# Performance work log

Hardware: AMD Instinct MI355X
Metric: run time of the kernel (lower is better)

## Reference

```python
import jax, jax.numpy as jnp
import numpy as np

TEMP = 0.02
KD_W = 1.0
VSD_W = 1.0
VLAD_W = 1.0
CON_W = 1.0
MSE_W = 1.0

B, SS, ST, DS, DT, V, NV, NT = 8, 96, 128, 1024, 2048, 32000, 32, 64


def hungarian(cost):
    # Shortest-augmenting-path assignment (e-maxx / Jonker-Volgenant style).
    # Square cost [n, n]; returns col_of_row so that row i matches column
    # col_of_row[i] with minimal total cost (same as scipy linear_sum_assignment).
    cost = np.asarray(cost, dtype=np.float64)
    n = cost.shape[0]
    INF = 1e18
    u = np.zeros(n + 1)
    v = np.zeros(n + 1)
    p = np.zeros(n + 1, dtype=np.int64)
    way = np.zeros(n + 1, dtype=np.int64)
    for i in range(1, n + 1):
        p[0] = i
        j0 = 0
        minv = np.full(n + 1, INF)
        used = np.zeros(n + 1, dtype=bool)
        while True:
            used[j0] = True
            i0 = p[j0]
            js = np.nonzero(~used)[0]
            js = js[js > 0]
            cur = cost[i0 - 1, js - 1] - u[i0] - v[js]
            upd = cur < minv[js]
            minv[js] = np.where(upd, cur, minv[js])
            way[js] = np.where(upd, j0, way[js])
            k = int(np.argmin(minv[js]))
            delta = minv[js][k]
            j1 = int(js[k])
            u[p[used]] += delta
            v[used] -= delta
            minv[~used] -= delta
            j0 = j1
            if p[j0] == 0:
                break
        while j0:
            j1 = int(way[j0])
            p[j0] = p[j1]
            j0 = j1
    col_of_row = np.zeros(n, dtype=np.int64)
    for j in range(1, n + 1):
        col_of_row[p[j] - 1] = j - 1
    return col_of_row


def _match(s_logits, t_logits):
    # Per-sample L1 (p=1 cdist) cost between teacher rows and student cols,
    # then Hungarian matching. Host-side loop is unavoidable (sequential
    # combinatorial algorithm), matching the original per-sample scipy loop.
    idx = []
    for b in range(s_logits.shape[0]):
        cost = np.abs(t_logits[b][:, None, :] - s_logits[b][None, :, :]).sum(-1)
        idx.append(hungarian(cost))
    return np.stack(idx)


def _cosine(a, b, eps=1e-8):
    # a: [B, M, D], b: [B, N, D] -> [B, M, N]; torch F.cosine_similarity semantics
    an = a / jnp.maximum(jnp.linalg.norm(a, axis=-1, keepdims=True), eps)
    bn = b / jnp.maximum(jnp.linalg.norm(b, axis=-1, keepdims=True), eps)
    return jnp.einsum('bmd,bnd->bmn', an, bn)


def setup_inputs() -> dict:
    key = jax.random.key(0)
    ks = jax.random.split(key, 12)
    f = jax.random.normal
    return {
        's_qry_reps': f(ks[0], (B, DS), jnp.float32),
        's_pos_reps': f(ks[1], (B, DS), jnp.float32),
        't_qry_reps': f(ks[2], (B, DT), jnp.float32),
        't_pos_reps': f(ks[3], (B, DT), jnp.float32),
        's_hidden_qry': f(ks[4], (B, SS, DS), jnp.float32),
        's_hidden_pos': f(ks[5], (B, SS, DS), jnp.float32),
        't_hidden_qry': f(ks[6], (B, ST, DT), jnp.float32),
        't_hidden_pos': f(ks[7], (B, ST, DT), jnp.float32),
        'W_s_lm': f(ks[8], (DS, V), jnp.float32) / np.float32(np.sqrt(DS)),
        'W_t_lm': f(ks[9], (DT, V), jnp.float32) / np.float32(np.sqrt(DT)),
        'W_proj': f(ks[10], (DT, DS), jnp.float32) / np.float32(np.sqrt(DT)),
        'b_proj': jnp.zeros((DS,), jnp.float32),
        'nv': NV,
        'nt': NT,
    }


def reference(s_qry_reps, s_pos_reps, t_qry_reps, t_pos_reps,
              s_hidden_qry, s_hidden_pos, t_hidden_qry, t_hidden_pos,
              W_s_lm, W_t_lm, W_proj, b_proj, nv, nt):
    Bn = s_qry_reps.shape[0]
    # 1) contrastive InfoNCE (world_size=1 -> gather is identity, target=arange)
    scores = (s_qry_reps @ s_pos_reps.T) / TEMP
    logp = jax.nn.log_softmax(scores, axis=-1)
    contrastive = -jnp.mean(jnp.diagonal(logp))
    # 2) MSE vs t2s-projected teacher reps
    mse = 0.5 * (jnp.mean((s_qry_reps - (t_qry_reps @ W_proj + b_proj)) ** 2)
                 + jnp.mean((s_pos_reps - (t_pos_reps @ W_proj + b_proj)) ** 2))
    # 3/4) VSD + VLAD over qry and pos sides stacked -> [2B, ...]
    s_hid = jnp.concatenate([s_hidden_qry, s_hidden_pos], axis=0)
    t_hid = jnp.concatenate([t_hidden_qry, t_hidden_pos], axis=0)
    St = t_hid.shape[1]
    sv = s_hid[:, :nv]                      # student vision tokens   [2B, Nv, DS]
    st = s_hid[:, nv:nv + nt]               # student text tokens     [2B, Nt, DS]
    tv = t_hid[:, St - nv - nt:St - nt]     # teacher vision tokens   [2B, Nv, DT]
    tt = t_hid[:, St - nt:]                 # teacher text tokens     [2B, Nt, DT]
    s_logits = jnp.einsum('bnd,dv->bnv', sv, W_s_lm)   # [2B, Nv, V]
    t_logits = jnp.einsum('bnd,dv->bnv', tv, W_t_lm)   # [2B, Nv, V]
    # Hungarian matching on detached logits (host side, like the original)
    idx = jnp.asarray(_match(np.asarray(s_logits), np.asarray(t_logits)))  # [2B, Nv]
    # VSD: MSE between matched student logits and teacher logits (t order = arange)
    s_logits_m = jnp.take_along_axis(s_logits, idx[:, :, None], axis=1)
    vsd = jnp.sum(jnp.mean((s_logits_m - t_logits) ** 2, axis=(1, 2)))
    # VLAD: smooth-L1 on vision->text cosine affinity maps
    sv_m = jnp.take_along_axis(sv, idx[:, :, None], axis=1)
    d = _cosine(sv_m, st) - _cosine(tv, tt)            # [2B, Nv, Nt]
    ad = jnp.abs(d)
    sl1 = jnp.where(ad < 1.0, 0.5 * d * d, ad - 0.5)
    vlad = jnp.sum(jnp.mean(sl1, axis=(1, 2)))
    distill = (VSD_W * vsd + VLAD_W * vlad) / Bn
    loss = CON_W * contrastive + MSE_W * mse + KD_W * distill
    return loss, contrastive, distill
```

## Files before the change

### kernel.cpp

```cpp
#include <hip/hip_runtime.h>
#include <math.h>

#define DS_ 1024
#define DT_ 2048
#define V_  32000
#define SS_ 96
#define ST_ 128


__device__ __forceinline__ float block_reduce_sum_256(float v) {
  __shared__ float tmp[4];
  #pragma unroll
  for (int off = 32; off; off >>= 1) v += __shfl_xor(v, off);
  const int wid = threadIdx.x >> 6;
  if ((threadIdx.x & 63) == 0) tmp[wid] = v;
  __syncthreads();
  if (threadIdx.x == 0) v = tmp[0] + tmp[1] + tmp[2] + tmp[3];
  return v;
}

__device__ __forceinline__ const float* s_base(int b, const float* s_hq, const float* s_hp) {
  return (b < 8) ? (s_hq + (size_t)b * SS_ * DS_) : (s_hp + (size_t)(b - 8) * SS_ * DS_);
}
__device__ __forceinline__ const float* t_base(int b, const float* t_hq, const float* t_hp) {
  return (b < 8) ? (t_hq + (size_t)b * ST_ * DT_) : (t_hp + (size_t)(b - 8) * ST_ * DT_);
}

__device__ __forceinline__ unsigned short f2bf(float x) {
  unsigned int u = __float_as_uint(x);
  u += 0x7fffu + ((u >> 16) & 1u);
  return (unsigned short)(u >> 16);
}
__device__ __forceinline__ float bf2f(unsigned short u) {
  return __uint_as_float(((unsigned int)u) << 16);
}

using bf16x8 = __attribute__((ext_vector_type(8))) short;
using f32x4  = __attribute__((ext_vector_type(4))) float;
using u16x4  = __attribute__((ext_vector_type(4))) unsigned short;

__device__ __forceinline__ void gll16(const void* g, void* l) {
  __builtin_amdgcn_global_load_lds((const __attribute__((address_space(1))) unsigned int*)g,
                                   (__attribute__((address_space(3))) unsigned int*)l, 16, 0, 0);
}

__device__ __forceinline__ unsigned int wave_umin_dpp(unsigned int r) {
  unsigned int t;
  t = (unsigned int)__builtin_amdgcn_update_dpp((int)r, (int)r, 0x111, 0xF, 0xF, false); r = r < t ? r : t;
  t = (unsigned int)__builtin_amdgcn_update_dpp((int)r, (int)r, 0x112, 0xF, 0xF, false); r = r < t ? r : t;
  t = (unsigned int)__builtin_amdgcn_update_dpp((int)r, (int)r, 0x114, 0xF, 0xF, false); r = r < t ? r : t;
  t = (unsigned int)__builtin_amdgcn_update_dpp((int)r, (int)r, 0x118, 0xF, 0xF, false); r = r < t ? r : t;
  t = (unsigned int)__builtin_amdgcn_update_dpp((int)r, (int)r, 0x142, 0xF, 0xF, false); r = r < t ? r : t;
  t = (unsigned int)__builtin_amdgcn_update_dpp((int)r, (int)r, 0x143, 0xF, 0xF, false); r = r < t ? r : t;
  return r;
}


__global__ __launch_bounds__(256) void scores_kernel(const float* __restrict__ sq,
                                                     const float* __restrict__ sp,
                                                     float* __restrict__ scores) {
  const int i = blockIdx.x >> 3, j = blockIdx.x & 7;
  float acc = 0.f;
  for (int k = threadIdx.x; k < DS_; k += 256)
    acc += sq[(size_t)i * DS_ + k] * sp[(size_t)j * DS_ + k];
  acc = block_reduce_sum_256(acc);
  if (threadIdx.x == 0) scores[i * 8 + j] = acc * 50.0f;
}


__global__ __launch_bounds__(256) void proj2_kernel(const float* __restrict__ t_qry,
                                                    const float* __restrict__ t_pos,
                                                    const float* __restrict__ Wp,
                                                    float* __restrict__ proj) {
  __shared__ float tv[16][64];
  const int kc = blockIdx.x;
  const int tid = threadIdx.x;
  for (int s = tid; s < 16 * 64; s += 256) {
    const int zi = s >> 6, k = s & 63;
    const float* t = (zi >= 8) ? (t_pos + (size_t)(zi - 8) * DT_) : (t_qry + (size_t)zi * DT_);
    tv[zi][k] = t[kc * 64 + k];
  }
  __syncthreads();
  const int d4 = tid * 4;
  float4 acc[16];
  #pragma unroll
  for (int zi = 0; zi < 16; ++zi) acc[zi] = (float4){0.f, 0.f, 0.f, 0.f};
  for (int k = 0; k < 64; ++k) {
    const float4 w = *(const float4*)&Wp[(size_t)(kc * 64 + k) * DS_ + d4];
    #pragma unroll
    for (int zi = 0; zi < 16; ++zi) {
      const float t = tv[zi][k];
      acc[zi].x += t * w.x; acc[zi].y += t * w.y;
      acc[zi].z += t * w.z; acc[zi].w += t * w.w;
    }
  }
  #pragma unroll
  for (int zi = 0; zi < 16; ++zi) {
    float* p = proj + (size_t)zi * DS_ + d4;
    atomicAdd(&p[0], acc[zi].x); atomicAdd(&p[1], acc[zi].y);
    atomicAdd(&p[2], acc[zi].z); atomicAdd(&p[3], acc[zi].w);
  }
}


__global__ __launch_bounds__(256) void mse2_kernel(const float* __restrict__ s_qry,
                                                   const float* __restrict__ s_pos,
                                                   const float* __restrict__ proj,
                                                   const float* __restrict__ bp,
                                                   float* __restrict__ mse_acc) {
  const int z = blockIdx.x >> 3, i = blockIdx.x & 7;
  const float* s = (z ? s_pos : s_qry) + (size_t)i * DS_;
  const float* p = proj + ((size_t)z * 8 + i) * DS_;
  float ss = 0.f;
  for (int d = threadIdx.x; d < DS_; d += 256) {
    const float diff = s[d] - (p[d] + bp[d]);
    ss += diff * diff;
  }
  ss = block_reduce_sum_256(ss);
  if (threadIdx.x == 0) atomicAdd(mse_acc, ss);
}


__global__ __launch_bounds__(256) void pack_as_kernel(const float* __restrict__ s_hq,
                                                      const float* __restrict__ s_hp,
                                                      unsigned short* __restrict__ As) {
  const int g = blockIdx.x;
  const int b = g >> 5, i = g & 31;
  const float* src = s_base(b, s_hq, s_hp) + (size_t)i * DS_;
  const int k4 = threadIdx.x * 4;
  const float4 w = *(const float4*)&src[k4];
  u16x4 o; o[0] = f2bf(w.x); o[1] = f2bf(w.y); o[2] = f2bf(w.z); o[3] = f2bf(w.w);
  *(u16x4*)&As[(size_t)g * DS_ + k4] = o;
}

__global__ __launch_bounds__(256) void pack_at_kernel(const float* __restrict__ t_hq,
                                                      const float* __restrict__ t_hp,
                                                      unsigned short* __restrict__ At) {
  const int g = blockIdx.x;
  const int b = g >> 5, i = g & 31;
  const float* src = t_base(b, t_hq, t_hp) + (size_t)(32 + i) * DT_;
  #pragma unroll
  for (int it = 0; it < 2; ++it) {
    const int k4 = (threadIdx.x + it * 256) * 4;
    const float4 w = *(const float4*)&src[k4];
    u16x4 o; o[0] = f2bf(w.x); o[1] = f2bf(w.y); o[2] = f2bf(w.z); o[3] = f2bf(w.w);
    *(u16x4*)&At[(size_t)g * DT_ + k4] = o;
  }
}

__global__ __launch_bounds__(256) void convw_kernel(const float* __restrict__ W,
                                                    unsigned short* __restrict__ Wbt,
                                                    int K) {
  __shared__ float tile[64][65];
  const int v0 = blockIdx.x * 64, k0 = blockIdx.y * 64;
  const int tid = threadIdx.x;
  #pragma unroll
  for (int it = 0; it < 4; ++it) {
    const int kr = (tid >> 4) + it * 16;
    const int v4 = (tid & 15) * 4;
    const float4 w = *(const float4*)&W[(size_t)(k0 + kr) * V_ + v0 + v4];
    tile[v4 + 0][kr] = w.x; tile[v4 + 1][kr] = w.y;
    tile[v4 + 2][kr] = w.z; tile[v4 + 3][kr] = w.w;
  }
  __syncthreads();
  #pragma unroll
  for (int it = 0; it < 2; ++it) {
    const int s = tid + it * 256;
    const int v = s >> 3, ch = s & 7;
    const float* src = &tile[v][ch * 8];
    unsigned int o[4];
    #pragma unroll
    for (int q = 0; q < 4; ++q)
      o[q] = (unsigned int)f2bf(src[2 * q]) | ((unsigned int)f2bf(src[2 * q + 1]) << 16);
    uint4 pk = {o[0], o[1], o[2], o[3]};
    *(uint4*)&Wbt[(size_t)(v0 + v) * K + k0 + ch * 8] = pk;
  }
}


template <int K>
__global__ __launch_bounds__(256) void gemm_tn_kernel(const unsigned short* __restrict__ A,
                                                      const unsigned short* __restrict__ Wbt,
                                                      unsigned short* __restrict__ Out) {
  __shared__ __align__(16) unsigned short Alds[2][256 * 32];
  __shared__ __align__(16) unsigned short Blds[2][128 * 32];
  const int nwg = gridDim.x;
  const int q = nwg >> 3, r = nwg & 7;
  const int xcd = blockIdx.x & 7, off = blockIdx.x >> 3;
  const int blk = (xcd < r ? xcd * (q + 1) : r * (q + 1) + (xcd - r) * q) + off;
  const int m0 = (blk & 1) * 256;
  const int n0 = (blk >> 1) * 128;
  const int tid = threadIdx.x;
  const int wv = tid >> 6, lane = tid & 63;
  const int lr = lane & 15, cc = lane >> 4;

  f32x4 acc[4][8];
  #pragma unroll
  for (int mf = 0; mf < 4; ++mf)
    #pragma unroll
    for (int nf = 0; nf < 8; ++nf) acc[mf][nf] = (f32x4){0.f, 0.f, 0.f, 0.f};

  constexpr int NT = K / 32;

  auto stage = [&](int kt, int buf) {
    #pragma unroll
    for (int it = 0; it < 4; ++it) {
      const int slot = it * 256 + tid;
      const int row = slot >> 2, cs = slot & 3;
      gll16(A + (size_t)(m0 + row) * K + kt * 32 + ((cs ^ ((row >> 1) & 3)) << 3),
            Alds[buf] + (size_t)(it * 256 + wv * 64) * 8);
    }
    #pragma unroll
    for (int it = 0; it < 2; ++it) {
      const int slot = it * 256 + tid;
      const int row = slot >> 2, cs = slot & 3;
      gll16(Wbt + (size_t)(n0 + row) * K + kt * 32 + ((cs ^ ((row >> 1) & 3)) << 3),
            Blds[buf] + (size_t)(it * 256 + wv * 64) * 8);
    }
  };

  stage(0, 0);
  if (NT > 1) stage(1, 1);
  for (int kt = 0; kt < NT; ++kt) {
    const int cur = kt & 1;
    if (kt >= 1 && kt + 1 < NT) stage(kt + 1, cur ^ 1);
    if (kt + 1 < NT) asm volatile("s_waitcnt vmcnt(6)" ::: "memory");
    else             asm volatile("s_waitcnt vmcnt(0)" ::: "memory");
    asm volatile("s_barrier" ::: "memory");
    bf16x8 af[4];
    #pragma unroll
    for (int mf = 0; mf < 4; ++mf) {
      const int row = wv * 64 + mf * 16 + lr;
      af[mf] = *(const bf16x8*)(Alds[cur] + row * 32 + ((cc ^ ((row >> 1) & 3)) << 3));
    }
    __builtin_amdgcn_s_setprio(1);
    #pragma unroll
    for (int nf = 0; nf < 8; ++nf) {
      const int vr = nf * 16 + lr;
      const bf16x8 bfr = *(const bf16x8*)(Blds[cur] + vr * 32 + ((cc ^ ((vr >> 1) & 3)) << 3));
      #pragma unroll
      for (int mf = 0; mf < 4; ++mf)
        acc[mf][nf] = __builtin_amdgcn_mfma_f32_16x16x32_bf16(af[mf], bfr, acc[mf][nf], 0, 0, 0);
    }
    __builtin_amdgcn_s_setprio(0);
    asm volatile("s_barrier" ::: "memory");
  }

  unsigned short* Olds = &Alds[0][0];
  #pragma unroll
  for (int h = 0; h < 2; ++h) {
    if (h) __syncthreads();
    #pragma unroll
    for (int mf = 0; mf < 4; ++mf)
      #pragma unroll
      for (int nf4 = 0; nf4 < 4; ++nf4) {
        const int nf = h * 4 + nf4;
        #pragma unroll
        for (int q2 = 0; q2 < 4; ++q2) {
          const int row = wv * 64 + mf * 16 + (lane >> 4) * 4 + q2;
          const int col = nf4 * 16 + lr;
          Olds[row * 64 + (col ^ (((row >> 2) & 3) << 4))] = f2bf(acc[mf][nf][q2]);
        }
      }
    __syncthreads();
    #pragma unroll
    for (int it = 0; it < 4; ++it) {
      const int slot = it * 256 + tid;
      const int row = slot >> 3, c2 = slot & 7;
      const uint4 pk = *(const uint4*)&Olds[row * 64 + ((c2 ^ (((row >> 2) & 3) << 1)) << 3)];
      *(uint4*)&Out[(size_t)(m0 + row) * V_ + n0 + h * 64 + c2 * 8] = pk;
    }
  }
}


#define CPV 500
#define CPP 508

__global__ __launch_bounds__(256) void cost_pairs_kernel(const unsigned short* __restrict__ Sg,
                                                         const unsigned short* __restrict__ Tg,
                                                         float* __restrict__ cost1,
                                                         float* __restrict__ cost2) {
  __shared__ __align__(16) unsigned short Sl[32 * CPP];
  __shared__ __align__(16) unsigned short Tl[32 * CPP];
  const int b = blockIdx.x >> 6, sl = blockIdx.x & 63;
  const int v0 = sl * CPV;
  const int tid = threadIdx.x;

  for (int s = tid; s < 32 * 125; s += 256) {
    const int r = s / 125, c = s % 125;
    *(u16x4*)&Sl[r * CPP + c * 4] = *(const u16x4*)&Sg[(size_t)(b * 32 + r) * V_ + v0 + c * 4];
    *(u16x4*)&Tl[r * CPP + c * 4] = *(const u16x4*)&Tg[(size_t)(b * 32 + r) * V_ + v0 + c * 4];
  }
  __syncthreads();

  const int i = tid >> 3, j4 = (tid & 7) * 4;
  float a1[4] = {0.f, 0.f, 0.f, 0.f}, a2[4] = {0.f, 0.f, 0.f, 0.f};
  for (int v = 0; v < CPV; v += 4) {
    const u16x4 t4 = *(const u16x4*)&Tl[i * CPP + v];
    float tf[4];
    #pragma unroll
    for (int q = 0; q < 4; ++q) tf[q] = bf2f(t4[q]);
    #pragma unroll
    for (int jj = 0; jj < 4; ++jj) {
      const u16x4 s4 = *(const u16x4*)&Sl[(j4 + jj) * CPP + v];
      #pragma unroll
      for (int q = 0; q < 4; ++q) {
        const float d = tf[q] - bf2f(s4[q]);
        a1[jj] += fabsf(d);
        a2[jj] += d * d;
      }
    }
  }
  #pragma unroll
  for (int jj = 0; jj < 4; ++jj) {
    atomicAdd(&cost1[(size_t)b * 1024 + i * 32 + j4 + jj], a1[jj]);
    atomicAdd(&cost2[(size_t)b * 1024 + i * 32 + j4 + jj], a2[jj]);
  }
}


__global__ __launch_bounds__(64) void hungarian_kernel(const float* __restrict__ cost1,
                                                       const float* __restrict__ cost2,
                                                       int* __restrict__ idx,
                                                       float* __restrict__ vsd_acc) {
  const int b = blockIdx.x;
  const int lane = threadIdx.x;
  const float INF = __int_as_float(0x7f800000);
  __shared__ float C[32 * 33];
  __shared__ float u_lds[33];

  for (int s = lane; s < 1024; s += 64) {
    const int r = s >> 5, c = s & 31;
    C[r * 33 + c] = cost1[(size_t)b * 1024 + s];
  }
  if (lane == 0) u_lds[0] = 0.f;
  __syncthreads();

  const bool isj = (lane >= 1 && lane <= 32);
  const int cix = isj ? (lane - 1) : 0;

  if (lane < 32) {
    float m = C[lane * 33];
    for (int j = 1; j < 32; ++j) m = fminf(m, C[lane * 33 + j]);
    u_lds[lane + 1] = m;
  }
  __syncthreads();

  float v = 0.f;
  if (isj) {
    float m = INF;
    for (int i = 0; i < 32; ++i) m = fminf(m, C[i * 33 + cix] - u_lds[i + 1]);
    v = m;
  }

  int p = 0;
  unsigned int assigned = 0;
  for (int i = 1; i <= 32; ++i) {
    const float ui = u_lds[i];
    const bool zero = isj && (p == 0) && ((C[(i - 1) * 33 + cix] - ui) == v);
    const unsigned long long tie = __ballot(zero);
    if (tie) {
      const int j1 = __ffsll(tie) - 1;
      if (lane == j1) p = i;
      assigned |= (1u << (i - 1));
    }
  }

  for (int i = 1; i <= 32; ++i) {
    if (assigned & (1u << (i - 1))) continue;
    if (lane == 0) p = i;
    float minv = INF;
    int way = 0;
    int used = 0;
    int j0 = 0;
    float ui0 = u_lds[i];
    float crow = C[(i - 1) * 33 + cix];
    while (true) {
      if (lane == j0) used = 1;
      float val = INF;
      if (isj && !used) {
        const float cur = crow - ui0 - v;
        if (cur < minv) { minv = cur; way = j0; }
        val = minv;
      }
      const unsigned int rb = wave_umin_dpp(__float_as_uint(val));
      const unsigned int minb = (unsigned int)__builtin_amdgcn_readlane((int)rb, 63);
      const float delta = __uint_as_float(minb);
      const unsigned long long tie = __ballot(__float_as_uint(val) == minb);
      const int j1 = __ffsll(tie) - 1;
      const int i0n = __builtin_amdgcn_readlane(p, j1);
      const float ui0n = u_lds[i0n];
      const int nri = (i0n >= 1 ? i0n : 1) - 1;
      const float cnext = C[nri * 33 + cix];
      if (used) {
        u_lds[p] += delta;
        v -= delta;
      } else {
        minv -= delta;
      }
      j0 = j1;
      if (i0n == 0) break;
      ui0 = ui0n;
      crow = cnext;
    }
    while (j0) {
      const int j1 = __builtin_amdgcn_readlane(way, j0);
      const int pv = __builtin_amdgcn_readlane(p, j1);
      if (lane == j0) p = pv;
      j0 = j1;
    }
  }
  float term = 0.f;
  if (isj) {
    idx[b * 32 + (p - 1)] = lane - 1;
    term = cost2[(size_t)b * 1024 + (p - 1) * 32 + (lane - 1)];
  }
  #pragma unroll
  for (int off = 32; off; off >>= 1) term += __shfl_xor(term, off);
  if (lane == 0) atomicAdd(vsd_acc, term);
}


__global__ __launch_bounds__(256) void norms_kernel(const float* __restrict__ s_hq,
                                                    const float* __restrict__ s_hp,
                                                    const float* __restrict__ t_hq,
                                                    const float* __restrict__ t_hp,
                                                    float* __restrict__ invn) {
  const int blk = blockIdx.x;
  const int b = blk / 192, t = blk % 192;
  const float* bs = s_base(b, s_hq, s_hp);
  const float* bt = t_base(b, t_hq, t_hp);
  const float* row;
  int K;
  float* out;
  if (t < 32)       { row = bs + (size_t)t * DS_;             K = DS_; out = invn + b * 32 + t; }
  else if (t < 96)  { row = bs + (size_t)t * DS_;             K = DS_; out = invn + 512 + b * 64 + (t - 32); }
  else if (t < 128) { row = bt + (size_t)(t - 96 + 32) * DT_;  K = DT_; out = invn + 1536 + b * 32 + (t - 96); }
  else              { row = bt + (size_t)(t - 128 + 64) * DT_; K = DT_; out = invn + 2048 + b * 64 + (t - 128); }
  float ss = 0.f;
  for (int k = threadIdx.x; k < K; k += 256) { const float x = row[k]; ss += x * x; }
  ss = block_reduce_sum_256(ss);
  if (threadIdx.x == 0) *out = 1.0f / fmaxf(sqrtf(ss), 1e-8f);
}


__global__ __launch_bounds__(256) void vlad_kernel2(const float* __restrict__ s_hq,
                                                    const float* __restrict__ s_hp,
                                                    const float* __restrict__ t_hq,
                                                    const float* __restrict__ t_hp,
                                                    const int* __restrict__ idx,
                                                    const float* __restrict__ invn,
                                                    float* __restrict__ vlad_acc) {
  const int b = blockIdx.x >> 5, i = blockIdx.x & 31;
  const int wv = threadIdx.x >> 6, lane = threadIdx.x & 63;
  const float* bs = s_base(b, s_hq, s_hp);
  const float* bt = t_base(b, t_hq, t_hp);
  const int is = idx[b * 32 + i];
  const float* a1p = bs + (size_t)is * DS_;
  const float* a2p = bt + (size_t)(32 + i) * DT_;
  float a1[16], a2[32];
  #pragma unroll
  for (int q = 0; q < 16; ++q) a1[q] = a1p[lane + 64 * q];
  #pragma unroll
  for (int q = 0; q < 32; ++q) a2[q] = a2p[lane + 64 * q];
  const float in_s = invn[b * 32 + is];
  const float in_t = invn[1536 + b * 32 + i];
  float local = 0.f;
  for (int jj = 0; jj < 16; ++jj) {
    const int j = wv * 16 + jj;
    const float* b1 = bs + (size_t)(32 + j) * DS_;
    const float* b2 = bt + (size_t)(64 + j) * DT_;
    float ds = 0.f, dt = 0.f;
    #pragma unroll
    for (int q = 0; q < 16; ++q) ds += a1[q] * b1[lane + 64 * q];
    #pragma unroll
    for (int q = 0; q < 32; ++q) dt += a2[q] * b2[lane + 64 * q];
    #pragma unroll
    for (int off = 32; off; off >>= 1) {
      ds += __shfl_xor(ds, off);
      dt += __shfl_xor(dt, off);
    }
    if (lane == 0) {
      const float cs = ds * in_s * invn[512 + b * 64 + j];
      const float ct = dt * in_t * invn[2048 + b * 64 + j];
      const float d = cs - ct;
      const float ad = fabsf(d);
      local += (ad < 1.f) ? 0.5f * d * d : ad - 0.5f;
    }
  }
  if (lane == 0) atomicAdd(vlad_acc, local);
}


__global__ __launch_bounds__(64) void final_kernel(const float* __restrict__ scores,
                                                   const float* __restrict__ accs,
                                                   float* __restrict__ out) {
  const int lane = threadIdx.x;
  float ci = 0.f;
  if (lane < 8) {
    float m = -1e30f;
    for (int j = 0; j < 8; ++j) m = fmaxf(m, scores[lane * 8 + j]);
    float sum = 0.f;
    for (int j = 0; j < 8; ++j) sum += expf(scores[lane * 8 + j] - m);
    const float lse = m + logf(sum);
    ci = scores[lane * 8 + lane] - lse;
  }
  #pragma unroll
  for (int off = 32; off; off >>= 1) ci += __shfl_xor(ci, off);
  if (lane == 0) {
    const float contrastive = -ci / 8.0f;
    const float mse = accs[0] / 16384.0f;
    const float vsd = accs[1] / 1024000.0f;
    const float vlad = accs[2] / 2048.0f;
    const float distill = (vsd + vlad) / 8.0f;
    out[0] = contrastive + mse + distill;
    out[1] = contrastive;
    out[2] = distill;
  }
}


extern "C" void kernel_launch(void* const* d_in, const int* in_sizes, int n_in,
                              void* d_out, int out_size, void* d_ws, size_t ws_size,
                              hipStream_t stream) {
  const float* s_qry = (const float*)d_in[0];
  const float* s_pos = (const float*)d_in[1];
  const float* t_qry = (const float*)d_in[2];
  const float* t_pos = (const float*)d_in[3];
  const float* s_hq  = (const float*)d_in[4];
  const float* s_hp  = (const float*)d_in[5];
  const float* t_hq  = (const float*)d_in[6];
  const float* t_hp  = (const float*)d_in[7];
  const float* Ws    = (const float*)d_in[8];
  const float* Wt    = (const float*)d_in[9];
  const float* Wp    = (const float*)d_in[10];
  const float* bp    = (const float*)d_in[11];

  float* ws     = (float*)d_ws;
  float* scores = ws;
  float* cost1  = ws + 64;
  float* cost2  = ws + 16448;
  float* invn   = ws + 32832;
  float* accs   = ws + 35904;
  float* proj   = ws + 35908;
  int*   idx    = (int*)(ws + 52292);
  const size_t small_bytes = (size_t)(52292 + 512) * 4;

  const size_t As_off = 262144;
  const size_t At_off = As_off + (size_t)512 * DS_ * 2;
  const size_t Ws_off = At_off + (size_t)512 * DT_ * 2;
  const size_t Wt_off = Ws_off + (size_t)V_ * DS_ * 2;
  const size_t Sg_off = Wt_off + (size_t)V_ * DT_ * 2;
  const size_t Tg_off = Sg_off + (size_t)512 * V_ * 2;
  const size_t req2   = Tg_off + (size_t)512 * V_ * 2;

  hipMemsetAsync(d_ws, 0, small_bytes, stream);

  scores_kernel<<<64, 256, 0, stream>>>(s_qry, s_pos, scores);
  proj2_kernel<<<32, 256, 0, stream>>>(t_qry, t_pos, Wp, proj);
  mse2_kernel<<<16, 256, 0, stream>>>(s_qry, s_pos, proj, bp, accs + 0);
  norms_kernel<<<16 * 192, 256, 0, stream>>>(s_hq, s_hp, t_hq, t_hp, invn);

  if (ws_size >= req2) {
    unsigned short* As  = (unsigned short*)((char*)d_ws + As_off);
    unsigned short* At  = (unsigned short*)((char*)d_ws + At_off);
    unsigned short* Wsb = (unsigned short*)((char*)d_ws + Ws_off);
    unsigned short* Wtb = (unsigned short*)((char*)d_ws + Wt_off);
    unsigned short* Sg  = (unsigned short*)((char*)d_ws + Sg_off);
    unsigned short* Tg  = (unsigned short*)((char*)d_ws + Tg_off);
    pack_as_kernel<<<512, 256, 0, stream>>>(s_hq, s_hp, As);
    pack_at_kernel<<<512, 256, 0, stream>>>(t_hq, t_hp, At);
    convw_kernel<<<dim3(V_ / 64, DS_ / 64), 256, 0, stream>>>(Ws, Wsb, DS_);
    convw_kernel<<<dim3(V_ / 64, DT_ / 64), 256, 0, stream>>>(Wt, Wtb, DT_);
    gemm_tn_kernel<DS_><<<(V_ / 128) * 2, 256, 0, stream>>>(As, Wsb, Sg);
    gemm_tn_kernel<DT_><<<(V_ / 128) * 2, 256, 0, stream>>>(At, Wtb, Tg);
    cost_pairs_kernel<<<16 * 64, 256, 0, stream>>>(Sg, Tg, cost1, cost2);
  }

  hungarian_kernel<<<16, 64, 0, stream>>>(cost1, cost2, idx, accs + 1);
  vlad_kernel2<<<512, 256, 0, stream>>>(s_hq, s_hp, t_hq, t_hp, idx, invn, accs + 2);
  final_kernel<<<1, 64, 0, stream>>>(scores, accs, (float*)d_out);
}
```

Measured before the change: 508.1 us.

## Fuse prep and mid-stage kernels into multi-role launches and precompute teacher cosines

Merges scores, projection, norms, packing and the student weight conversion into one heterogeneous kernel indexed by block range. A second kernel runs the student GEMM, the teacher weight conversion and the teacher cosine dot products side by side. The teacher vision-text cosine matrix is computed once, before the Hungarian step, so the VLAD kernel only has to do the student side. This removes several launch gaps and runs independent work concurrently, at the cost of larger shared-memory reservations per block and uneven block roles. The final kernels now also sit inside the workspace-size branch.

Result: faster. 463.8 us (-8.7%).

```diff
diff --git a/kernel.cpp b/kernel.cpp
--- a/kernel.cpp
+++ b/kernel.cpp
@@ -56,10 +56,10 @@
 }
 
 
-__global__ __launch_bounds__(256) void scores_kernel(const float* __restrict__ sq,
-                                                     const float* __restrict__ sp,
-                                                     float* __restrict__ scores) {
-  const int i = blockIdx.x >> 3, j = blockIdx.x & 7;
+__device__ __forceinline__ void scores_body(int blk, const float* __restrict__ sq,
+                                            const float* __restrict__ sp,
+                                            float* __restrict__ scores) {
+  const int i = blk >> 3, j = blk & 7;
   float acc = 0.f;
   for (int k = threadIdx.x; k < DS_; k += 256)
     acc += sq[(size_t)i * DS_ + k] * sp[(size_t)j * DS_ + k];
@@ -67,13 +67,12 @@
   if (threadIdx.x == 0) scores[i * 8 + j] = acc * 50.0f;
 }
 
-
-__global__ __launch_bounds__(256) void proj2_kernel(const float* __restrict__ t_qry,
-                                                    const float* __restrict__ t_pos,
-                                                    const float* __restrict__ Wp,
-                                                    float* __restrict__ proj) {
-  __shared__ float tv[16][64];
-  const int kc = blockIdx.x;
+__device__ __forceinline__ void proj2_body(int kc, const float* __restrict__ t_qry,
+                                           const float* __restrict__ t_pos,
+                                           const float* __restrict__ Wp,
+                                           float* __restrict__ proj,
+                                           unsigned char* smem) {
+  float (*tv)[64] = (float (*)[64])smem;
   const int tid = threadIdx.x;
   for (int s = tid; s < 16 * 64; s += 256) {
     const int zi = s >> 6, k = s & 63;
@@ -100,6 +99,252 @@
     atomicAdd(&p[0], acc[zi].x); atomicAdd(&p[1], acc[zi].y);
     atomicAdd(&p[2], acc[zi].z); atomicAdd(&p[3], acc[zi].w);
   }
+}
+
+__device__ __forceinline__ void norms_body(int blk, const float* __restrict__ s_hq,
+                                           const float* __restrict__ s_hp,
+                                           const float* __restrict__ t_hq,
+                                           const float* __restrict__ t_hp,
+                                           float* __restrict__ invn) {
+  const int b = blk / 192, t = blk % 192;
+  const float* bs = s_base(b, s_hq, s_hp);
+  const float* bt = t_base(b, t_hq, t_hp);
+  const float* row;
+  int K;
+  float* out;
+  if (t < 32)       { row = bs + (size_t)t * DS_;             K = DS_; out = invn + b * 32 + t; }
+  else if (t < 96)  { row = bs + (size_t)t * DS_;             K = DS_; out = invn + 512 + b * 64 + (t - 32); }
+  else if (t < 128) { row = bt + (size_t)(t - 96 + 32) * DT_;  K = DT_; out = invn + 1536 + b * 32 + (t - 96); }
+  else              { row = bt + (size_t)(t - 128 + 64) * DT_; K = DT_; out = invn + 2048 + b * 64 + (t - 128); }
+  float ss = 0.f;
+  for (int k = threadIdx.x; k < K; k += 256) { const float x = row[k]; ss += x * x; }
+  ss = block_reduce_sum_256(ss);
+  if (threadIdx.x == 0) *out = 1.0f / fmaxf(sqrtf(ss), 1e-8f);
+}
+
+__device__ __forceinline__ void pack_as_body(int g, const float* __restrict__ s_hq,
+                                             const float* __restrict__ s_hp,
+                                             unsigned short* __restrict__ As) {
+  const int b = g >> 5, i = g & 31;
+  const float* src = s_base(b, s_hq, s_hp) + (size_t)i * DS_;
+  const int k4 = threadIdx.x * 4;
+  const float4 w = *(const float4*)&src[k4];
+  u16x4 o; o[0] = f2bf(w.x); o[1] = f2bf(w.y); o[2] = f2bf(w.z); o[3] = f2bf(w.w);
+  *(u16x4*)&As[(size_t)g * DS_ + k4] = o;
+}
+
+__device__ __forceinline__ void pack_at_body(int g, const float* __restrict__ t_hq,
+                                             const float* __restrict__ t_hp,
+                                             unsigned short* __restrict__ At) {
+  const int b = g >> 5, i = g & 31;
+  const float* src = t_base(b, t_hq, t_hp) + (size_t)(32 + i) * DT_;
+  #pragma unroll
+  for (int it = 0; it < 2; ++it) {
+    const int k4 = (threadIdx.x + it * 256) * 4;
+    const float4 w = *(const float4*)&src[k4];
+    u16x4 o; o[0] = f2bf(w.x); o[1] = f2bf(w.y); o[2] = f2bf(w.z); o[3] = f2bf(w.w);
+    *(u16x4*)&At[(size_t)g * DT_ + k4] = o;
+  }
+}
+
+__device__ __forceinline__ void convw_body(int id, const float* __restrict__ W,
+                                           unsigned short* __restrict__ Wbt,
+                                           int K, unsigned char* smem) {
+  float (*tile)[65] = (float (*)[65])smem;
+  const int v0 = (id % 500) * 64, k0 = (id / 500) * 64;
+  const int tid = threadIdx.x;
+  #pragma unroll
+  for (int it = 0; it < 4; ++it) {
+    const int kr = (tid >> 4) + it * 16;
+    const int v4 = (tid & 15) * 4;
+    const float4 w = *(const float4*)&W[(size_t)(k0 + kr) * V_ + v0 + v4];
+    tile[v4 + 0][kr] = w.x; tile[v4 + 1][kr] = w.y;
+    tile[v4 + 2][kr] = w.z; tile[v4 + 3][kr] = w.w;
+  }
+  __syncthreads();
+  #pragma unroll
+  for (int it = 0; it < 2; ++it) {
+    const int s = tid + it * 256;
+    const int v = s >> 3, ch = s & 7;
+    const float* src = &tile[v][ch * 8];
+    unsigned int o[4];
+    #pragma unroll
+    for (int q = 0; q < 4; ++q)
+      o[q] = (unsigned int)f2bf(src[2 * q]) | ((unsigned int)f2bf(src[2 * q + 1]) << 16);
+    uint4 pk = {o[0], o[1], o[2], o[3]};
+    *(uint4*)&Wbt[(size_t)(v0 + v) * K + k0 + ch * 8] = pk;
+  }
+}
+
+__device__ __forceinline__ void dt_body(int id, const float* __restrict__ t_hq,
+                                        const float* __restrict__ t_hp,
+                                        const float* __restrict__ invn,
+                                        float* __restrict__ ct) {
+  const int b = id >> 5, i = id & 31;
+  const int wv = threadIdx.x >> 6, lane = threadIdx.x & 63;
+  const float* bt = t_base(b, t_hq, t_hp);
+  const float* a2p = bt + (size_t)(32 + i) * DT_;
+  float a2[32];
+  #pragma unroll
+  for (int q = 0; q < 32; ++q) a2[q] = a2p[lane + 64 * q];
+  const float in_t = invn[1536 + b * 32 + i];
+  for (int jj = 0; jj < 16; ++jj) {
+    const int j = wv * 16 + jj;
+    const float* b2 = bt + (size_t)(64 + j) * DT_;
+    float dt = 0.f;
+    #pragma unroll
+    for (int q = 0; q < 32; ++q) dt += a2[q] * b2[lane + 64 * q];
+    #pragma unroll
+    for (int off = 32; off; off >>= 1) dt += __shfl_xor(dt, off);
+    if (lane == 0) ct[(b * 32 + i) * 64 + j] = dt * in_t * invn[2048 + b * 64 + j];
+  }
+}
+
+
+template <int K>
+__device__ __forceinline__ void gemm_body(int blk, int nwg,
+                                          const unsigned short* __restrict__ A,
+                                          const unsigned short* __restrict__ Wbt,
+                                          unsigned short* __restrict__ Out,
+                                          unsigned char* smem) {
+  unsigned short* AldsB = (unsigned short*)smem;
+  unsigned short* BldsB = (unsigned short*)(smem + 32768);
+  const int q = nwg >> 3, r = nwg & 7;
+  const int xcd = blk & 7, off = blk >> 3;
+  const int sblk = (xcd < r ? xcd * (q + 1) : r * (q + 1) + (xcd - r) * q) + off;
+  const int m0 = (sblk & 1) * 256;
+  const int n0 = (sblk >> 1) * 128;
+  const int tid = threadIdx.x;
+  const int wv = tid >> 6, lane = tid & 63;
+  const int lr = lane & 15, cc = lane >> 4;
+
+  f32x4 acc[4][8];
+  #pragma unroll
+  for (int mf = 0; mf < 4; ++mf)
+    #pragma unroll
+    for (int nf = 0; nf < 8; ++nf) acc[mf][nf] = (f32x4){0.f, 0.f, 0.f, 0.f};
+
+  constexpr int NT = K / 32;
+
+  auto stage = [&](int kt, int buf) {
+    #pragma unroll
+    for (int it = 0; it < 4; ++it) {
+      const int slot = it * 256 + tid;
+      const int row = slot >> 2, cs = slot & 3;
+      gll16(A + (size_t)(m0 + row) * K + kt * 32 + ((cs ^ ((row >> 1) & 3)) << 3),
+            AldsB + (size_t)buf * 8192 + (size_t)(it * 256 + wv * 64) * 8);
+    }
+    #pragma unroll
+    for (int it = 0; it < 2; ++it) {
+      const int slot = it * 256 + tid;
+      const int row = slot >> 2, cs = slot & 3;
+      gll16(Wbt + (size_t)(n0 + row) * K + kt * 32 + ((cs ^ ((row >> 1) & 3)) << 3),
+            BldsB + (size_t)buf * 4096 + (size_t)(it * 256 + wv * 64) * 8);
+    }
+  };
+
+  stage(0, 0);
+  if (NT > 1) stage(1, 1);
+  for (int kt = 0; kt < NT; ++kt) {
+    const int cur = kt & 1;
+    if (kt >= 1 && kt + 1 < NT) stage(kt + 1, cur ^ 1);
+    if (kt + 1 < NT) asm volatile("s_waitcnt vmcnt(6)" ::: "memory");
+    else             asm volatile("s_waitcnt vmcnt(0)" ::: "memory");
+    asm volatile("s_barrier" ::: "memory");
+    bf16x8 af[4];
+    #pragma unroll
+    for (int mf = 0; mf < 4; ++mf) {
+      const int row = wv * 64 + mf * 16 + lr;
+      af[mf] = *(const bf16x8*)(AldsB + cur * 8192 + row * 32 + ((cc ^ ((row >> 1) & 3)) << 3));
+    }
+    __builtin_amdgcn_s_setprio(1);
+    #pragma unroll
+    for (int nf = 0; nf < 8; ++nf) {
+      const int vr = nf * 16 + lr;
+      const bf16x8 bfr = *(const bf16x8*)(BldsB + cur * 4096 + vr * 32 + ((cc ^ ((vr >> 1) & 3)) << 3));
+      #pragma unroll
+      for (int mf = 0; mf < 4; ++mf)
+        acc[mf][nf] = __builtin_amdgcn_mfma_f32_16x16x32_bf16(af[mf], bfr, acc[mf][nf], 0, 0, 0);
+    }
+    __builtin_amdgcn_s_setprio(0);
+    asm volatile("s_barrier" ::: "memory");
+  }
+
+  unsigned short* Olds = AldsB;
+  #pragma unroll
+  for (int h = 0; h < 2; ++h) {
+    if (h) __syncthreads();
+    #pragma unroll
+    for (int mf = 0; mf < 4; ++mf)
+      #pragma unroll
+      for (int nf4 = 0; nf4 < 4; ++nf4) {
+        const int nf = h * 4 + nf4;
+        #pragma unroll
+        for (int q2 = 0; q2 < 4; ++q2) {
+          const int row = wv * 64 + mf * 16 + (lane >> 4) * 4 + q2;
+          const int col = nf4 * 16 + lr;
+          Olds[row * 64 + (col ^ (((row >> 2) & 3) << 4))] = f2bf(acc[mf][nf][q2]);
+        }
+      }
+    __syncthreads();
+    #pragma unroll
+    for (int it = 0; it < 4; ++it) {
+      const int slot = it * 256 + tid;
+      const int row = slot >> 3, c2 = slot & 7;
+      const uint4 pk = *(const uint4*)&Olds[row * 64 + ((c2 ^ (((row >> 2) & 3) << 1)) << 3)];
+      *(uint4*)&Out[(size_t)(m0 + row) * V_ + n0 + h * 64 + c2 * 8] = pk;
+    }
+  }
+}
+
+
+__global__ __launch_bounds__(256) void fused_pre_kernel(const float* __restrict__ s_qry,
+                                                        const float* __restrict__ s_pos,
+                                                        const float* __restrict__ t_qry,
+                                                        const float* __restrict__ t_pos,
+                                                        const float* __restrict__ s_hq,
+                                                        const float* __restrict__ s_hp,
+                                                        const float* __restrict__ t_hq,
+                                                        const float* __restrict__ t_hp,
+                                                        const float* __restrict__ Ws,
+                                                        const float* __restrict__ Wp,
+                                                        float* __restrict__ scores,
+                                                        float* __restrict__ proj,
+                                                        float* __restrict__ invn,
+                                                        unsigned short* __restrict__ As,
+                                                        unsigned short* __restrict__ At,
+                                                        unsigned short* __restrict__ Wsb) {
+  __shared__ __align__(16) unsigned char smem[16640];
+  const int blk = blockIdx.x;
+  if (blk < 64)            scores_body(blk, s_qry, s_pos, scores);
+  else if (blk < 96)       proj2_body(blk - 64, t_qry, t_pos, Wp, proj, smem);
+  else if (blk < 3168)     norms_body(blk - 96, s_hq, s_hp, t_hq, t_hp, invn);
+  else if (blk < 3680)     pack_as_body(blk - 3168, s_hq, s_hp, As);
+  else if (blk < 4192)     pack_at_body(blk - 3680, t_hq, t_hp, At);
+  else                     convw_body(blk - 4192, Ws, Wsb, DS_, smem);
+}
+
+__global__ __launch_bounds__(256) void fused_mid_kernel(const unsigned short* __restrict__ As,
+                                                        const unsigned short* __restrict__ Wsb,
+                                                        unsigned short* __restrict__ Sg,
+                                                        const float* __restrict__ Wt,
+                                                        unsigned short* __restrict__ Wtb,
+                                                        const float* __restrict__ t_hq,
+                                                        const float* __restrict__ t_hp,
+                                                        const float* __restrict__ invn,
+                                                        float* __restrict__ ct) {
+  __shared__ __align__(16) unsigned char smem[49152];
+  const int blk = blockIdx.x;
+  if (blk < 500)            gemm_body<DS_>(blk, 500, As, Wsb, Sg, smem);
+  else if (blk < 16500)     convw_body(blk - 500, Wt, Wtb, DT_, smem);
+  else                      dt_body(blk - 16500, t_hq, t_hp, invn, ct);
+}
+
+__global__ __launch_bounds__(256) void gemm_tn_kernel_t(const unsigned short* __restrict__ A,
+                                                        const unsigned short* __restrict__ Wbt,
+                                                        unsigned short* __restrict__ Out) {
+  __shared__ __align__(16) unsigned char smem[49152];
+  gemm_body<DT_>(blockIdx.x, (int)gridDim.x, A, Wbt, Out, smem);
 }
 
 
@@ -118,159 +363,6 @@
   }
   ss = block_reduce_sum_256(ss);
   if (threadIdx.x == 0) atomicAdd(mse_acc, ss);
-}
-
-
-__global__ __launch_bounds__(256) void pack_as_kernel(const float* __restrict__ s_hq,
-                                                      const float* __restrict__ s_hp,
-                                                      unsigned short* __restrict__ As) {
-  const int g = blockIdx.x;
-  const int b = g >> 5, i = g & 31;
-  const float* src = s_base(b, s_hq, s_hp) + (size_t)i * DS_;
-  const int k4 = threadIdx.x * 4;
-  const float4 w = *(const float4*)&src[k4];
-  u16x4 o; o[0] = f2bf(w.x); o[1] = f2bf(w.y); o[2] = f2bf(w.z); o[3] = f2bf(w.w);
-  *(u16x4*)&As[(size_t)g * DS_ + k4] = o;
-}
-
-__global__ __launch_bounds__(256) void pack_at_kernel(const float* __restrict__ t_hq,
-                                                      const float* __restrict__ t_hp,
-                                                      unsigned short* __restrict__ At) {
-  const int g = blockIdx.x;
-  const int b = g >> 5, i = g & 31;
-  const float* src = t_base(b, t_hq, t_hp) + (size_t)(32 + i) * DT_;
-  #pragma unroll
-  for (int it = 0; it < 2; ++it) {
-    const int k4 = (threadIdx.x + it * 256) * 4;
-    const float4 w = *(const float4*)&src[k4];
-    u16x4 o; o[0] = f2bf(w.x); o[1] = f2bf(w.y); o[2] = f2bf(w.z); o[3] = f2bf(w.w);
-    *(u16x4*)&At[(size_t)g * DT_ + k4] = o;
-  }
-}
-
-__global__ __launch_bounds__(256) void convw_kernel(const float* __restrict__ W,
-                                                    unsigned short* __restrict__ Wbt,
-                                                    int K) {
-  __shared__ float tile[64][65];
-  const int v0 = blockIdx.x * 64, k0 = blockIdx.y * 64;
-  const int tid = threadIdx.x;
-  #pragma unroll
-  for (int it = 0; it < 4; ++it) {
-    const int kr = (tid >> 4) + it * 16;
-    const int v4 = (tid & 15) * 4;
-    const float4 w = *(const float4*)&W[(size_t)(k0 + kr) * V_ + v0 + v4];
-    tile[v4 + 0][kr] = w.x; tile[v4 + 1][kr] = w.y;
-    tile[v4 + 2][kr] = w.z; tile[v4 + 3][kr] = w.w;
-  }
-  __syncthreads();
-  #pragma unroll
-  for (int it = 0; it < 2; ++it) {
-    const int s = tid + it * 256;
-    const int v = s >> 3, ch = s & 7;
-    const float* src = &tile[v][ch * 8];
-    unsigned int o[4];
-    #pragma unroll
-    for (int q = 0; q < 4; ++q)
-      o[q] = (unsigned int)f2bf(src[2 * q]) | ((unsigned int)f2bf(src[2 * q + 1]) << 16);
-    uint4 pk = {o[0], o[1], o[2], o[3]};
-    *(uint4*)&Wbt[(size_t)(v0 + v) * K + k0 + ch * 8] = pk;
-  }
-}
-
-
-template <int K>
-__global__ __launch_bounds__(256) void gemm_tn_kernel(const unsigned short* __restrict__ A,
-                                                      const unsigned short* __restrict__ Wbt,
-                                                      unsigned short* __restrict__ Out) {
-  __shared__ __align__(16) unsigned short Alds[2][256 * 32];
-  __shared__ __align__(16) unsigned short Blds[2][128 * 32];
-  const int nwg = gridDim.x;
-  const int q = nwg >> 3, r = nwg & 7;
-  const int xcd = blockIdx.x & 7, off = blockIdx.x >> 3;
-  const int blk = (xcd < r ? xcd * (q + 1) : r * (q + 1) + (xcd - r) * q) + off;
-  const int m0 = (blk & 1) * 256;
-  const int n0 = (blk >> 1) * 128;
-  const int tid = threadIdx.x;
-  const int wv = tid >> 6, lane = tid & 63;
-  const int lr = lane & 15, cc = lane >> 4;
-
-  f32x4 acc[4][8];
-  #pragma unroll
-  for (int mf = 0; mf < 4; ++mf)
-    #pragma unroll
-    for (int nf = 0; nf < 8; ++nf) acc[mf][nf] = (f32x4){0.f, 0.f, 0.f, 0.f};
-
-  constexpr int NT = K / 32;
-
-  auto stage = [&](int kt, int buf) {
-    #pragma unroll
-    for (int it = 0; it < 4; ++it) {
-      const int slot = it * 256 + tid;
-      const int row = slot >> 2, cs = slot & 3;
-      gll16(A + (size_t)(m0 + row) * K + kt * 32 + ((cs ^ ((row >> 1) & 3)) << 3),
-            Alds[buf] + (size_t)(it * 256 + wv * 64) * 8);
-    }
-    #pragma unroll
-    for (int it = 0; it < 2; ++it) {
-      const int slot = it * 256 + tid;
-      const int row = slot >> 2, cs = slot & 3;
-      gll16(Wbt + (size_t)(n0 + row) * K + kt * 32 + ((cs ^ ((row >> 1) & 3)) << 3),
-            Blds[buf] + (size_t)(it * 256 + wv * 64) * 8);
-    }
-  };
-
-  stage(0, 0);
-  if (NT > 1) stage(1, 1);
-  for (int kt = 0; kt < NT; ++kt) {
-    const int cur = kt & 1;
-    if (kt >= 1 && kt + 1 < NT) stage(kt + 1, cur ^ 1);
-    if (kt + 1 < NT) asm volatile("s_waitcnt vmcnt(6)" ::: "memory");
-    else             asm volatile("s_waitcnt vmcnt(0)" ::: "memory");
-    asm volatile("s_barrier" ::: "memory");
-    bf16x8 af[4];
-    #pragma unroll
-    for (int mf = 0; mf < 4; ++mf) {
-      const int row = wv * 64 + mf * 16 + lr;
-      af[mf] = *(const bf16x8*)(Alds[cur] + row * 32 + ((cc ^ ((row >> 1) & 3)) << 3));
-    }
-    __builtin_amdgcn_s_setprio(1);
-    #pragma unroll
-    for (int nf = 0; nf < 8; ++nf) {
-      const int vr = nf * 16 + lr;
-      const bf16x8 bfr = *(const bf16x8*)(Blds[cur] + vr * 32 + ((cc ^ ((vr >> 1) & 3)) << 3));
-      #pragma unroll
-      for (int mf = 0; mf < 4; ++mf)
-        acc[mf][nf] = __builtin_amdgcn_mfma_f32_16x16x32_bf16(af[mf], bfr, acc[mf][nf], 0, 0, 0);
-    }
-    __builtin_amdgcn_s_setprio(0);
-    asm volatile("s_barrier" ::: "memory");
-  }
-
-  unsigned short* Olds = &Alds[0][0];
-  #pragma unroll
-  for (int h = 0; h < 2; ++h) {
-    if (h) __syncthreads();
-    #pragma unroll
-    for (int mf = 0; mf < 4; ++mf)
-      #pragma unroll
-      for (int nf4 = 0; nf4 < 4; ++nf4) {
-        const int nf = h * 4 + nf4;
-        #pragma unroll
-        for (int q2 = 0; q2 < 4; ++q2) {
-          const int row = wv * 64 + mf * 16 + (lane >> 4) * 4 + q2;
-          const int col = nf4 * 16 + lr;
-          Olds[row * 64 + (col ^ (((row >> 2) & 3) << 4))] = f2bf(acc[mf][nf][q2]);
-        }
-      }
-    __syncthreads();
-    #pragma unroll
-    for (int it = 0; it < 4; ++it) {
-      const int slot = it * 256 + tid;
-      const int row = slot >> 3, c2 = slot & 7;
-      const uint4 pk = *(const uint4*)&Olds[row * 64 + ((c2 ^ (((row >> 2) & 3) << 1)) << 3)];
-      *(uint4*)&Out[(size_t)(m0 + row) * V_ + n0 + h * 64 + c2 * 8] = pk;
-    }
-  }
 }
 
 
@@ -422,69 +514,33 @@
 }
 
 
-__global__ __launch_bounds__(256) void norms_kernel(const float* __restrict__ s_hq,
-                                                    const float* __restrict__ s_hp,
-                                                    const float* __restrict__ t_hq,
-                                                    const float* __restrict__ t_hp,
-                                                    float* __restrict__ invn) {
-  const int blk = blockIdx.x;
-  const int b = blk / 192, t = blk % 192;
-  const float* bs = s_base(b, s_hq, s_hp);
-  const float* bt = t_base(b, t_hq, t_hp);
-  const float* row;
-  int K;
-  float* out;
-  if (t < 32)       { row = bs + (size_t)t * DS_;             K = DS_; out = invn + b * 32 + t; }
-  else if (t < 96)  { row = bs + (size_t)t * DS_;             K = DS_; out = invn + 512 + b * 64 + (t - 32); }
-  else if (t < 128) { row = bt + (size_t)(t - 96 + 32) * DT_;  K = DT_; out = invn + 1536 + b * 32 + (t - 96); }
-  else              { row = bt + (size_t)(t - 128 + 64) * DT_; K = DT_; out = invn + 2048 + b * 64 + (t - 128); }
-  float ss = 0.f;
-  for (int k = threadIdx.x; k < K; k += 256) { const float x = row[k]; ss += x * x; }
-  ss = block_reduce_sum_256(ss);
-  if (threadIdx.x == 0) *out = 1.0f / fmaxf(sqrtf(ss), 1e-8f);
-}
-
-
-__global__ __launch_bounds__(256) void vlad_kernel2(const float* __restrict__ s_hq,
-                                                    const float* __restrict__ s_hp,
-                                                    const float* __restrict__ t_hq,
-                                                    const float* __restrict__ t_hp,
-                                                    const int* __restrict__ idx,
-                                                    const float* __restrict__ invn,
-                                                    float* __restrict__ vlad_acc) {
+__global__ __launch_bounds__(256) void vlad_final_kernel(const float* __restrict__ s_hq,
+                                                         const float* __restrict__ s_hp,
+                                                         const int* __restrict__ idx,
+                                                         const float* __restrict__ invn,
+                                                         const float* __restrict__ ct,
+                                                         float* __restrict__ vlad_acc) {
   const int b = blockIdx.x >> 5, i = blockIdx.x & 31;
   const int wv = threadIdx.x >> 6, lane = threadIdx.x & 63;
   const float* bs = s_base(b, s_hq, s_hp);
-  const float* bt = t_base(b, t_hq, t_hp);
   const int is = idx[b * 32 + i];
   const float* a1p = bs + (size_t)is * DS_;
-  const float* a2p = bt + (size_t)(32 + i) * DT_;
-  float a1[16], a2[32];
+  float a1[16];
   #pragma unroll
   for (int q = 0; q < 16; ++q) a1[q] = a1p[lane + 64 * q];
-  #pragma unroll
-  for (int q = 0; q < 32; ++q) a2[q] = a2p[lane + 64 * q];
   const float in_s = invn[b * 32 + is];
-  const float in_t = invn[1536 + b * 32 + i];
   float local = 0.f;
   for (int jj = 0; jj < 16; ++jj) {
     const int j = wv * 16 + jj;
     const float* b1 = bs + (size_t)(32 + j) * DS_;
-    const float* b2 = bt + (size_t)(64 + j) * DT_;
-    float ds = 0.f, dt = 0.f;
+    float ds = 0.f;
     #pragma unroll
     for (int q = 0; q < 16; ++q) ds += a1[q] * b1[lane + 64 * q];
     #pragma unroll
-    for (int q = 0; q < 32; ++q) dt += a2[q] * b2[lane + 64 * q];
-    #pragma unroll
-    for (int off = 32; off; off >>= 1) {
-      ds += __shfl_xor(ds, off);
-      dt += __shfl_xor(dt, off);
-    }
+    for (int off = 32; off; off >>= 1) ds += __shfl_xor(ds, off);
     if (lane == 0) {
       const float cs = ds * in_s * invn[512 + b * 64 + j];
-      const float ct = dt * in_t * invn[2048 + b * 64 + j];
-      const float d = cs - ct;
+      const float d = cs - ct[(b * 32 + i) * 64 + j];
       const float ad = fabsf(d);
       local += (ad < 1.f) ? 0.5f * d * d : ad - 0.5f;
     }
@@ -545,9 +601,10 @@
   float* accs   = ws + 35904;
   float* proj   = ws + 35908;
   int*   idx    = (int*)(ws + 52292);
-  const size_t small_bytes = (size_t)(52292 + 512) * 4;
-
-  const size_t As_off = 262144;
+  float* ct     = ws + 52804;
+  const size_t small_bytes = (size_t)52804 * 4;
+
+  const size_t As_off = 524288;
   const size_t At_off = As_off + (size_t)512 * DS_ * 2;
   const size_t Ws_off = At_off + (size_t)512 * DT_ * 2;
   const size_t Wt_off = Ws_off + (size_t)V_ * DS_ * 2;
@@ -556,11 +613,6 @@
   const size_t req2   = Tg_off + (size_t)512 * V_ * 2;
 
   hipMemsetAsync(d_ws, 0, small_bytes, stream);
-
-  scores_kernel<<<64, 256, 0, stream>>>(s_qry, s_pos, scores);
-  proj2_kernel<<<32, 256, 0, stream>>>(t_qry, t_pos, Wp, proj);
-  mse2_kernel<<<16, 256, 0, stream>>>(s_qry, s_pos, proj, bp, accs + 0);
-  norms_kernel<<<16 * 192, 256, 0, stream>>>(s_hq, s_hp, t_hq, t_hp, invn);
 
   if (ws_size >= req2) {
     unsigned short* As  = (unsigned short*)((char*)d_ws + As_off);
@@ -569,16 +621,20 @@
     unsigned short* Wtb = (unsigned short*)((char*)d_ws + Wt_off);
     unsigned short* Sg  = (unsigned short*)((char*)d_ws + Sg_off);
     unsigned short* Tg  = (unsigned short*)((char*)d_ws + Tg_off);
-    pack_as_kernel<<<512, 256, 0, stream>>>(s_hq, s_hp, As);
-    pack_at_kernel<<<512, 256, 0, stream>>>(t_hq, t_hp, At);
-    convw_kernel<<<dim3(V_ / 64, DS_ / 64), 256, 0, stream>>>(Ws, Wsb, DS_);
-    convw_kernel<<<dim3(V_ / 64, DT_ / 64), 256, 0, stream>>>(Wt, Wtb, DT_);
-    gemm_tn_kernel<DS_><<<(V_ / 128) * 2, 256, 0, stream>>>(As, Wsb, Sg);
-    gemm_tn_kernel<DT_><<<(V_ / 128) * 2, 256, 0, stream>>>(At, Wtb, Tg);
+
+    fused_pre_kernel<<<12192, 256, 0, stream>>>(s_qry, s_pos, t_qry, t_pos,
+                                                s_hq, s_hp, t_hq, t_hp,
+                                                Ws, Wp, scores, proj, invn, As, At, Wsb);
+    mse2_kernel<<<16, 256, 0, stream>>>(s_qry, s_pos, proj, bp, accs + 0);
+
+    fused_mid_kernel<<<17012, 256, 0, stream>>>(As, Wsb, Sg, Wt, Wtb,
+                                                t_hq, t_hp, invn, ct);
+
+    gemm_tn_kernel_t<<<(V_ / 128) * 2, 256, 0, stream>>>(At, Wtb, Tg);
     cost_pairs_kernel<<<16 * 64, 256, 0, stream>>>(Sg, Tg, cost1, cost2);
-  }
-
-  hungarian_kernel<<<16, 64, 0, stream>>>(cost1, cost2, idx, accs + 1);
-  vlad_kernel2<<<512, 256, 0, stream>>>(s_hq, s_hp, t_hq, t_hp, idx, invn, accs + 2);
-  final_kernel<<<1, 64, 0, stream>>>(scores, accs, (float*)d_out);
-}
+
+    hungarian_kernel<<<16, 64, 0, stream>>>(cost1, cost2, idx, accs + 1);
+    vlad_final_kernel<<<512, 256, 0, stream>>>(s_hq, s_hp, idx, invn, ct, accs + 2);
+    final_kernel<<<1, 64, 0, stream>>>(scores, accs, (float*)d_out);
+  }
+}
```
